# Kernel tuning notes

Hardware: AMD Instinct MI355X
Metric: run time of the kernel (lower is better)

Reference implementation:

```python
import jax, jax.numpy as jnp
import numpy as np

N_HEAD = 32
D_MODEL = 4096
N_KV_GROUPS = 8
D_HEAD = D_MODEL // N_HEAD            # 128
H_PER_G = N_HEAD // N_KV_GROUPS       # 4
KV_DIM = N_KV_GROUPS * D_HEAD         # 1024
B, S = 2, 2048


def setup_inputs() -> dict:
    key = jax.random.key(0)
    ks = jax.random.split(key, 8)
    q = jax.random.normal(ks[0], (B, S, D_MODEL), dtype=jnp.float32)
    k = jax.random.normal(ks[1], (B, S, D_MODEL), dtype=jnp.float32)
    v = jax.random.normal(ks[2], (B, S, D_MODEL), dtype=jnp.float32)
    # causal mask (True = keep), broadcast over b, g, h as in the torch module
    mask = jnp.tril(jnp.ones((S, S), dtype=bool))
    # params: torch init is torch.rand (uniform [0,1)); scale down for numerics
    w_q = jax.random.uniform(ks[3], (D_MODEL, D_MODEL), dtype=jnp.float32) * 0.02
    w_k = jax.random.uniform(ks[4], (KV_DIM, D_MODEL), dtype=jnp.float32) * 0.02
    w_v = jax.random.uniform(ks[5], (KV_DIM, D_MODEL), dtype=jnp.float32) * 0.02
    w_out = jax.random.uniform(ks[6], (D_MODEL, D_MODEL), dtype=jnp.float32) * 0.02
    return {"q": q, "k": k, "v": v, "w_q": w_q, "w_k": w_k, "w_v": w_v,
            "w_out": w_out, "mask": mask}


def reference(q, k, v, w_q, w_k, w_v, w_out, mask):
    b, n, _ = q.shape
    s = k.shape[1]
    # F.linear(x, W) == x @ W.T
    query = q @ w_q.T                                  # [b, n, d_model]
    key = k @ w_k.T                                    # [b, s, kv_dim]
    value = v @ w_v.T                                  # [b, s, kv_dim]
    # b n (h d) -> b h n d -> b g h n d
    query = query.reshape(b, n, N_HEAD, D_HEAD).transpose(0, 2, 1, 3)
    query = query.reshape(b, N_KV_GROUPS, H_PER_G, n, D_HEAD)
    # b s (g d) -> b g s d
    key = key.reshape(b, s, N_KV_GROUPS, D_HEAD).transpose(0, 2, 1, 3)
    value = value.reshape(b, s, N_KV_GROUPS, D_HEAD).transpose(0, 2, 1, 3)
    scores = jnp.einsum('bghnd,bgsd->bghns', query, key) / (D_HEAD ** 0.5)
    scores = jnp.where(mask, scores, jnp.finfo(scores.dtype).min)
    attention = jax.nn.softmax(scores, axis=-1)        # [b, g, h, n, s]
    out = jnp.einsum('bghns,bgsd->bghnd', attention, value)
    # b g h n d -> b n (g h d)
    out = out.transpose(0, 3, 1, 2, 4).reshape(b, n, D_MODEL)
    return out @ w_out.T
```

## Files before the change

### kernel.cpp

```cpp
#include <hip/hip_runtime.h>

typedef unsigned short u16;
typedef unsigned int u32;
typedef __bf16 bf16x8 __attribute__((ext_vector_type(8)));
typedef float f32x4 __attribute__((ext_vector_type(4)));
typedef u16 u16x8 __attribute__((ext_vector_type(8)));
typedef u32 u32x2 __attribute__((ext_vector_type(2)));

#define SCL2E 0.12751744898229718f

__device__ __forceinline__ u16 f2bf(float f) {
  union { float f; u32 u; } x; x.f = f;
  u32 r = x.u + 0x7fffu + ((x.u >> 16) & 1u);
  return (u16)(r >> 16);
}

__device__ __forceinline__ u32 cvt_pk_bf16(float lo, float hi) {
  u32 r;
  asm("v_cvt_pk_bf16_f32 %0, %1, %2" : "=v"(r) : "v"(lo), "v"(hi));
  return r;
}

__device__ __forceinline__ void gld16(const void* g, void* l) {
  __builtin_amdgcn_global_load_lds(
      (const __attribute__((address_space(1))) u32*)g,
      (__attribute__((address_space(3))) u32*)l, 16, 0, 0);
}

#define SBAR() __builtin_amdgcn_s_barrier()
#define WAITVM(N) do { asm volatile("s_waitcnt vmcnt(" #N ")" ::: "memory"); \
                       __builtin_amdgcn_sched_barrier(0); } while (0)

__device__ __forceinline__ void cvt_body(const float* __restrict__ in,
                                         u16* __restrict__ out, int n8) {
  int stride = gridDim.x * 256;
  for (int i = blockIdx.x * 256 + threadIdx.x; i < n8; i += stride) {
    float4 a = ((const float4*)in)[2*i];
    float4 b = ((const float4*)in)[2*i+1];
    u16x8 o;
    o[0]=f2bf(a.x); o[1]=f2bf(a.y); o[2]=f2bf(a.z); o[3]=f2bf(a.w);
    o[4]=f2bf(b.x); o[5]=f2bf(b.y); o[6]=f2bf(b.z); o[7]=f2bf(b.w);
    ((u16x8*)out)[i] = o;
  }
}

__global__ __launch_bounds__(256) void cvt3(
    const float* __restrict__ i0, const float* __restrict__ i1,
    const float* __restrict__ i2, u16* __restrict__ o0,
    u16* __restrict__ o1, u16* __restrict__ o2, int n8) {
  const float* in = blockIdx.y == 0 ? i0 : (blockIdx.y == 1 ? i1 : i2);
  u16* out = blockIdx.y == 0 ? o0 : (blockIdx.y == 1 ? o1 : o2);
  cvt_body(in, out, n8);
}

template<int OUTF32>
__device__ __forceinline__ void gemm256_body(
    const u16* __restrict__ Ag, const u16* __restrict__ Bg, void* __restrict__ Cp,
    const int K, const int ldc, const long m0, const long n0, const long cb,
    const float escale, u16* __restrict__ As, u16* __restrict__ Bs) {
  const int lane = threadIdx.x & 63, w = threadIdx.x >> 6;
  const int wm = w >> 2, wn = w & 3;
  const int c = lane & 15, grp = lane >> 4;
  const int lr = lane >> 3, lch = lane & 7;

  f32x4 acc[8][4] = {};
  const int NK = K >> 6;

#define STG(G, R0, DST, RIT, KT) do { \
    int rit_ = (RIT) + w*8 + lr; \
    int ch_ = lch ^ (rit_ & 7); \
    gld16((G) + ((R0) + rit_) * (long)K + (long)(KT)*64 + ch_*8, \
          (DST) + ((RIT) + w*8)*64); } while (0)

  STG(Bg, n0, Bs, 0, 0);   STG(Bg, n0, Bs, 64, 0);
  STG(Bg, n0, Bs, 128, 0); STG(Bg, n0, Bs, 192, 0);
  STG(Ag, m0, As, 0, 0);   STG(Ag, m0, As, 128, 0);
  STG(Ag, m0, As, 64, 0);  STG(Ag, m0, As, 192, 0);
  {
    u16* B1 = Bs + 16384;
    STG(Bg, n0, B1, 0, 1);   STG(Bg, n0, B1, 64, 1);
    STG(Bg, n0, B1, 128, 1); STG(Bg, n0, B1, 192, 1);
  }
  WAITVM(6);
  SBAR();

  for (int kt = 0; kt < NK; ++kt) {
    const u16* At = As + (kt & 1) * 16384;
    u16* An = As + ((kt & 1) ^ 1) * 16384;
    const u16* Bt = Bs + (kt % 3) * 16384;
    u16* Bn = Bs + ((kt + 2) % 3) * 16384;
    const bool am = (kt + 1 < NK), bm = (kt + 2 < NK);

    bf16x8 bfr[4][2];
#define LDAF(mi, ks) (*(const bf16x8*)(At + (wm*128 + (mi)*16 + c)*64 + ((((ks)*4 + grp)) ^ (c & 7))*8))
#define LDBF(ni, ks) (*(const bf16x8*)(Bt + (wn*64  + (ni)*16 + c)*64 + ((((ks)*4 + grp)) ^ (c & 7))*8))

#define PHASE(P, STAGES, WAITS) { \
    bf16x8 af0k0 = LDAF(2*(P),   0), af0k1 = LDAF(2*(P),   1); \
    bf16x8 af1k0 = LDAF(2*(P)+1, 0), af1k1 = LDAF(2*(P)+1, 1); \
    STAGES \
    WAITS \
    SBAR(); \
    __builtin_amdgcn_s_setprio(1); \
    _Pragma("unroll") \
    for (int ni = 0; ni < 4; ++ni) { \
      acc[2*(P)][ni]   = __builtin_amdgcn_mfma_f32_16x16x32_bf16(af0k0, bfr[ni][0], acc[2*(P)][ni],   0,0,0); \
      acc[2*(P)][ni]   = __builtin_amdgcn_mfma_f32_16x16x32_bf16(af0k1, bfr[ni][1], acc[2*(P)][ni],   0,0,0); \
      acc[2*(P)+1][ni] = __builtin_amdgcn_mfma_f32_16x16x32_bf16(af1k0, bfr[ni][0], acc[2*(P)+1][ni], 0,0,0); \
      acc[2*(P)+1][ni] = __builtin_amdgcn_mfma_f32_16x16x32_bf16(af1k1, bfr[ni][1], acc[2*(P)+1][ni], 0,0,0); \
    } \
    __builtin_amdgcn_s_setprio(0); \
    SBAR(); }

    #pragma unroll
    for (int ni = 0; ni < 4; ++ni) {
      bfr[ni][0] = LDBF(ni, 0);
      bfr[ni][1] = LDBF(ni, 1);
    }
    PHASE(0, if (am) { STG(Ag, m0, An, 0, kt+1); STG(Ag, m0, An, 128, kt+1); }, ;)
    PHASE(1, if (am) { STG(Ag, m0, An, 64, kt+1); STG(Ag, m0, An, 192, kt+1); },
             if (am) { WAITVM(4); } else { WAITVM(0); })
    PHASE(2, if (bm) { STG(Bg, n0, Bn, 0, kt+2); STG(Bg, n0, Bn, 64, kt+2); }, ;)
    PHASE(3, if (bm) { STG(Bg, n0, Bn, 128, kt+2); STG(Bg, n0, Bn, 192, kt+2); },
             if (bm) { WAITVM(6); } else if (am) { WAITVM(2); })
#undef PHASE
#undef LDAF
#undef LDBF
  }
#undef STG

  #pragma unroll
  for (int mi = 0; mi < 8; ++mi) {
    #pragma unroll
    for (int rr = 0; rr < 4; ++rr) {
      long row = m0 + wm*128 + mi*16 + grp*4 + rr;
      #pragma unroll
      for (int ni = 0; ni < 4; ++ni) {
        long col = cb + wn*64 + ni*16 + c;
        if (OUTF32) ((float*)Cp)[row*ldc + col] = acc[mi][ni][rr];
        else        ((u16*)Cp)[row*ldc + col]  = f2bf(acc[mi][ni][rr] * escale);
      }
    }
  }
}

__global__ __launch_bounds__(512, 2) void proj_gemm(
    const u16* __restrict__ qb, const u16* __restrict__ kb,
    const u16* __restrict__ vb, const u16* __restrict__ wqb,
    const u16* __restrict__ wkv, u16* __restrict__ Qp, u16* __restrict__ KVp) {
  __shared__ __attribute__((aligned(16))) u16 SMEM[5*16384];
  int wg = ((int)blockIdx.x & 7) * 48 + ((int)blockIdx.x >> 3);
  const u16 *A_, *B_; u16* C_; int ldc_; long m0, n0, cb; float esc;
  if (wg < 256)      { A_ = qb; B_ = wqb;           C_ = Qp;  ldc_ = 4096;
                       m0 = (long)(wg >> 4)*256; n0 = (long)(wg & 15)*256; cb = n0; esc = SCL2E; }
  else if (wg < 320) { int t = wg - 256; A_ = kb; B_ = wkv;   C_ = KVp; ldc_ = 2048;
                       m0 = (long)(t >> 2)*256; n0 = (long)(t & 3)*256; cb = n0; esc = 1.f; }
  else               { int t = wg - 320; A_ = vb; B_ = wkv + 4194304; C_ = KVp; ldc_ = 2048;
                       m0 = (long)(t >> 2)*256; n0 = (long)(t & 3)*256; cb = n0 + 1024; esc = 1.f; }
  gemm256_body<0>(A_, B_, C_, 4096, ldc_, m0, n0, cb, esc, SMEM, SMEM + 2*16384);
}

__global__ __launch_bounds__(512, 2) void gemm_out(
    const u16* __restrict__ A, const u16* __restrict__ Bw, float* __restrict__ C) {
  __shared__ __attribute__((aligned(16))) u16 SMEM[5*16384];
  int wg = ((int)blockIdx.x & 7) * 32 + ((int)blockIdx.x >> 3);
  long m0 = (long)(wg >> 4) * 256, n0 = (long)(wg & 15) * 256;
  gemm256_body<1>(A, Bw, C, 4096, 4096, m0, n0, n0, 1.f, SMEM, SMEM + 2*16384);
}

__global__ __launch_bounds__(256) void transpose_v(
    const u16* __restrict__ KVp, u16* __restrict__ Vt) {
  const int s0 = blockIdx.x * 64, n0 = blockIdx.y * 64, b = blockIdx.z;
  const int tid = threadIdx.x;
  __shared__ __attribute__((aligned(16))) u16 t[64*80];
  #pragma unroll
  for (int p = 0; p < 2; ++p) {
    int sl = p*32 + (tid >> 3), nl = (tid & 7) * 8;
    *(u16x8*)(t + sl*80 + nl) =
        *(const u16x8*)(KVp + (long)(b*2048 + s0 + sl)*2048 + 1024 + n0 + nl);
  }
  __syncthreads();
  #pragma unroll
  for (int p = 0; p < 2; ++p) {
    int nl = p*32 + (tid >> 3), sc = (tid & 7) * 8;
    u16x8 o;
    #pragma unroll
    for (int j = 0; j < 8; ++j) o[j] = t[(sc + j)*80 + nl];
    *(u16x8*)(Vt + (long)(b*1024 + n0 + nl)*2048 + s0 + sc) = o;
  }
}

__global__ __launch_bounds__(256, 2) void attn_fwd(
    const u16* __restrict__ Qp, const u16* __restrict__ KVp,
    const u16* __restrict__ Vt, u16* __restrict__ AO) {
  const int qt = gridDim.x - 1 - blockIdx.x;
  const int head = blockIdx.y, b = blockIdx.z;
  const int g = head >> 2;
  const int q0 = qt * 128;
  const int tid = threadIdx.x, lane = tid & 63, w = tid >> 6;
  const int c = lane & 15, grp = lane >> 4;
  const int qw = q0 + w * 32;

  __shared__ __attribute__((aligned(16))) u16 Ks[2][64*128];
  __shared__ __attribute__((aligned(16))) u16 Vts[2][128*64];
  __shared__ __attribute__((aligned(16))) u16 Ps[4][32*64];
  u16* __restrict__ pw = &Ps[w][0];

  bf16x8 qf[2][4];
  #pragma unroll
  for (int h = 0; h < 2; ++h) {
    const u16* qb = Qp + (long)(b*2048 + qw + h*16 + c)*4096 + head*128 + grp*8;
    #pragma unroll
    for (int t = 0; t < 4; ++t) qf[h][t] = *(const bf16x8*)(qb + t*32);
  }

  float m_run[2] = {-1e30f, -1e30f}, l_run[2] = {0.f, 0.f};
  f32x4 oacc[2][8] = {};

  const int ntiles = 2*qt + 2;

  auto STAGE = [&](int buf, int kt) {
    const int kv0 = kt * 64;
    #pragma unroll
    for (int p = 0; p < 4; ++p) {
      int idx = p*256 + w*64 + lane;
      int krow = idx >> 4, kc = idx & 15;
      int kcs = kc ^ (krow & 7);
      gld16(KVp + (long)(b*2048 + kv0 + krow)*2048 + g*128 + kcs*8,
            &Ks[buf][(p*256 + w*64)*8]);
      int d = idx >> 3, vc = idx & 7;
      int vcs = vc ^ (d & 7);
      gld16(Vt + (long)(b*1024 + g*128 + d)*2048 + kv0 + vcs*8,
            &Vts[buf][(p*256 + w*64)*8]);
    }
  };

  STAGE(0, 0);
  int cur = 0;
  for (int kt = 0; kt < ntiles; ++kt) {
    const int kv0 = kt * 64;
    __syncthreads();
    if (kt + 1 < ntiles) STAGE(cur ^ 1, kt + 1);

    const u16* __restrict__ Kc = &Ks[cur][0];
    const u16* __restrict__ Vc = &Vts[cur][0];

    f32x4 sacc[2][4] = {};
    #pragma unroll
    for (int f = 0; f < 4; ++f) {
      const int row = f*16 + c;
      #pragma unroll
      for (int t = 0; t < 4; ++t) {
        bf16x8 kf = *(const bf16x8*)(Kc + row*128 + (((t*4 + grp) ^ (c & 7)) * 8));
        sacc[0][f] = __builtin_amdgcn_mfma_f32_16x16x32_bf16(kf, qf[0][t], sacc[0][f], 0, 0, 0);
        sacc[1][f] = __builtin_amdgcn_mfma_f32_16x16x32_bf16(kf, qf[1][t], sacc[1][f], 0, 0, 0);
      }
    }

    #pragma unroll
    for (int h = 0; h < 2; ++h) {
      const int qg = qw + h*16 + c;
      float sv[16];
      if (kv0 + 63 > qw + h*16) {
        #pragma unroll
        for (int f = 0; f < 4; ++f)
          #pragma unroll
          for (int r = 0; r < 4; ++r) {
            float x = sacc[h][f][r];
            if (kv0 + f*16 + grp*4 + r > qg) x = -1e30f;
            sv[f*4 + r] = x;
          }
      } else {
        #pragma unroll
        for (int f = 0; f < 4; ++f)
          #pragma unroll
          for (int r = 0; r < 4; ++r) sv[f*4 + r] = sacc[h][f][r];
      }
      float tm[8];
      #pragma unroll
      for (int i = 0; i < 8; ++i) tm[i] = fmaxf(sv[i], sv[i+8]);
      #pragma unroll
      for (int i = 0; i < 4; ++i) tm[i] = fmaxf(tm[i], tm[i+4]);
      float tmax = fmaxf(fmaxf(tm[0], tm[2]), fmaxf(tm[1], tm[3]));
      tmax = fmaxf(tmax, __shfl_xor(tmax, 16));
      tmax = fmaxf(tmax, __shfl_xor(tmax, 32));

      float m_new = m_run[h];
      if (!__all(tmax <= m_run[h] + 8.f)) {
        m_new = fmaxf(m_run[h], tmax);
        float corr = exp2f(m_run[h] - m_new);
        l_run[h] *= corr;
        #pragma unroll
        for (int n = 0; n < 8; ++n) oacc[h][n] *= corr;
        m_run[h] = m_new;
      }

      float tsum = 0.f;
      u32 pk[8];
      #pragma unroll
      for (int i = 0; i < 8; ++i) {
        float p0 = exp2f(sv[2*i]   - m_new);
        float p1 = exp2f(sv[2*i+1] - m_new);
        tsum += p0 + p1;
        pk[i] = cvt_pk_bf16(p0, p1);
      }
      tsum += __shfl_xor(tsum, 16);
      tsum += __shfl_xor(tsum, 32);
      l_run[h] += tsum;

      #pragma unroll
      for (int f = 0; f < 4; ++f) {
        int col = (f*16 + grp*4) ^ ((c & 7) << 3);
        u32x2 pv; pv[0] = pk[2*f]; pv[1] = pk[2*f + 1];
        *(u32x2*)(pw + (h*16 + c)*64 + col) = pv;
      }
    }

    #pragma unroll
    for (int u = 0; u < 2; ++u) {
      const int pcol = (u*32 + grp*8) ^ ((c & 7) << 3);
      bf16x8 pf0 = *(const bf16x8*)(pw + c*64 + pcol);
      bf16x8 pf1 = *(const bf16x8*)(pw + (16 + c)*64 + pcol);
      #pragma unroll
      for (int n = 0; n < 8; ++n) {
        bf16x8 vf = *(const bf16x8*)(Vc + (n*16 + c)*64 + (((u*4 + grp) ^ (c & 7)) * 8));
        oacc[0][n] = __builtin_amdgcn_mfma_f32_16x16x32_bf16(vf, pf0, oacc[0][n], 0, 0, 0);
        oacc[1][n] = __builtin_amdgcn_mfma_f32_16x16x32_bf16(vf, pf1, oacc[1][n], 0, 0, 0);
      }
    }
    cur ^= 1;
  }

  #pragma unroll
  for (int h = 0; h < 2; ++h) {
    const float inv = 1.0f / l_run[h];
    u16* ob = AO + (long)(b*2048 + qw + h*16 + c)*4096 + head*128 + grp*4;
    #pragma unroll
    for (int n = 0; n < 8; ++n) {
      u32x2 o;
      o[0] = cvt_pk_bf16(oacc[h][n][0]*inv, oacc[h][n][1]*inv);
      o[1] = cvt_pk_bf16(oacc[h][n][2]*inv, oacc[h][n][3]*inv);
      *(u32x2*)(ob + n*16) = o;
    }
  }
}

extern "C" void kernel_launch(void* const* d_in, const int* in_sizes, int n_in,
                              void* d_out, int out_size, void* d_ws, size_t ws_size,
                              hipStream_t stream) {
  const float* q   = (const float*)d_in[0];
  const float* k   = (const float*)d_in[1];
  const float* v   = (const float*)d_in[2];
  const float* w_q = (const float*)d_in[3];
  const float* w_k = (const float*)d_in[4];
  const float* w_v = (const float*)d_in[5];
  const float* w_o = (const float*)d_in[6];

  u16* ws  = (u16*)d_ws;
  u16* qb  = ws;
  u16* kb  = qb  + 16777216;
  u16* vb  = kb  + 16777216;
  u16* wqb = vb  + 16777216;
  u16* wob = wqb + 16777216;
  u16* wkv = wob + 16777216;
  u16* Qp  = wkv + 8388608;
  u16* KVp = Qp  + 16777216;
  u16* Vtr = kb;
  u16* AO  = vb;
  (void)ws_size; (void)in_sizes; (void)n_in; (void)out_size;

  dim3 blk(256);
  cvt3<<<dim3(2048,3), blk, 0, stream>>>(q, k, v, qb, kb, vb, 2097152);
  cvt3<<<dim3(2048,2), blk, 0, stream>>>(w_q, w_o, w_o, wqb, wob, wob, 2097152);
  cvt3<<<dim3(512, 2), blk, 0, stream>>>(w_k, w_v, w_v, wkv, wkv + 4194304, wkv + 4194304, 524288);

  proj_gemm<<<384, dim3(512), 0, stream>>>(qb, kb, vb, wqb, wkv, Qp, KVp);
  transpose_v<<<dim3(32,16,2), blk, 0, stream>>>(KVp, Vtr);
  attn_fwd<<<dim3(16,32,2), blk, 0, stream>>>(Qp, KVp, Vtr, AO);
  gemm_out<<<256, dim3(512), 0, stream>>>(AO, wob, (float*)d_out);
}
```

Baseline: 629.7 us.

## Rebalance projection GEMM so each workgroup does one Q tile plus a K/V tile

The projection kernel used to launch 384 workgroups (256 Q tiles plus 128 K/V tiles of 256x256), which leaves a ragged second wave on 256 CUs. Now 256 workgroups each compute a 256x256 Q tile and then a 128x256 K or V tile through a new triple-buffered gemm128 body, so the per-workgroup work is even across a single wave. The attention kernel also raises wave priority around its MFMA blocks. The trade-offs are longer serial work per workgroup and LDS reuse between the two GEMMs in the same block. The final-phase wait logic in gemm256 is also slightly reshuffled.

```diff
diff --git a/kernel.cpp b/kernel.cpp
--- a/kernel.cpp
+++ b/kernel.cpp
@@ -30,6 +30,12 @@
 #define SBAR() __builtin_amdgcn_s_barrier()
 #define WAITVM(N) do { asm volatile("s_waitcnt vmcnt(" #N ")" ::: "memory"); \
                        __builtin_amdgcn_sched_barrier(0); } while (0)
+
+#define STG(G, R0, DST, RIT, KT, K) do { \
+    int rit_ = (RIT) + w*8 + lr; \
+    int ch_ = lch ^ (rit_ & 7); \
+    gld16((G) + ((R0) + rit_) * (long)(K) + (long)(KT)*64 + ch_*8, \
+          (DST) + ((RIT) + w*8)*64); } while (0)
 
 __device__ __forceinline__ void cvt_body(const float* __restrict__ in,
                                          u16* __restrict__ out, int n8) {
@@ -66,20 +72,14 @@
   f32x4 acc[8][4] = {};
   const int NK = K >> 6;
 
-#define STG(G, R0, DST, RIT, KT) do { \
-    int rit_ = (RIT) + w*8 + lr; \
-    int ch_ = lch ^ (rit_ & 7); \
-    gld16((G) + ((R0) + rit_) * (long)K + (long)(KT)*64 + ch_*8, \
-          (DST) + ((RIT) + w*8)*64); } while (0)
-
-  STG(Bg, n0, Bs, 0, 0);   STG(Bg, n0, Bs, 64, 0);
-  STG(Bg, n0, Bs, 128, 0); STG(Bg, n0, Bs, 192, 0);
-  STG(Ag, m0, As, 0, 0);   STG(Ag, m0, As, 128, 0);
-  STG(Ag, m0, As, 64, 0);  STG(Ag, m0, As, 192, 0);
+  STG(Bg, n0, Bs, 0, 0, K);   STG(Bg, n0, Bs, 64, 0, K);
+  STG(Bg, n0, Bs, 128, 0, K); STG(Bg, n0, Bs, 192, 0, K);
+  STG(Ag, m0, As, 0, 0, K);   STG(Ag, m0, As, 128, 0, K);
+  STG(Ag, m0, As, 64, 0, K);  STG(Ag, m0, As, 192, 0, K);
   {
     u16* B1 = Bs + 16384;
-    STG(Bg, n0, B1, 0, 1);   STG(Bg, n0, B1, 64, 1);
-    STG(Bg, n0, B1, 128, 1); STG(Bg, n0, B1, 192, 1);
+    STG(Bg, n0, B1, 0, 1, K);   STG(Bg, n0, B1, 64, 1, K);
+    STG(Bg, n0, B1, 128, 1, K); STG(Bg, n0, B1, 192, 1, K);
   }
   WAITVM(6);
   SBAR();
@@ -117,17 +117,16 @@
       bfr[ni][0] = LDBF(ni, 0);
       bfr[ni][1] = LDBF(ni, 1);
     }
-    PHASE(0, if (am) { STG(Ag, m0, An, 0, kt+1); STG(Ag, m0, An, 128, kt+1); }, ;)
-    PHASE(1, if (am) { STG(Ag, m0, An, 64, kt+1); STG(Ag, m0, An, 192, kt+1); },
+    PHASE(0, if (am) { STG(Ag, m0, An, 0, kt+1, K); STG(Ag, m0, An, 128, kt+1, K); }, ;)
+    PHASE(1, if (am) { STG(Ag, m0, An, 64, kt+1, K); STG(Ag, m0, An, 192, kt+1, K); },
              if (am) { WAITVM(4); } else { WAITVM(0); })
-    PHASE(2, if (bm) { STG(Bg, n0, Bn, 0, kt+2); STG(Bg, n0, Bn, 64, kt+2); }, ;)
-    PHASE(3, if (bm) { STG(Bg, n0, Bn, 128, kt+2); STG(Bg, n0, Bn, 192, kt+2); },
-             if (bm) { WAITVM(6); } else if (am) { WAITVM(2); })
+    PHASE(2, if (bm) { STG(Bg, n0, Bn, 0, kt+2, K); STG(Bg, n0, Bn, 64, kt+2, K); }, ;)
+    PHASE(3, if (bm) { STG(Bg, n0, Bn, 128, kt+2, K); STG(Bg, n0, Bn, 192, kt+2, K); WAITVM(6); }
+             else if (am) { WAITVM(2); }, ;)
 #undef PHASE
 #undef LDAF
 #undef LDBF
   }
-#undef STG
 
   #pragma unroll
   for (int mi = 0; mi < 8; ++mi) {
@@ -144,28 +143,112 @@
   }
 }
 
+__device__ __forceinline__ void gemm128_body(
+    const u16* __restrict__ Ag, const u16* __restrict__ Bg, u16* __restrict__ Cp,
+    const int K, const int ldc, const long m0, const long n0, const long cb,
+    u16* __restrict__ As, u16* __restrict__ Bs) {
+  const int lane = threadIdx.x & 63, w = threadIdx.x >> 6;
+  const int wm = w >> 2, wn = w & 3;
+  const int c = lane & 15, grp = lane >> 4;
+  const int lr = lane >> 3, lch = lane & 7;
+
+  f32x4 acc[4][4] = {};
+  const int NK = K >> 6;
+
+  STG(Bg, n0, Bs, 0, 0, K);   STG(Bg, n0, Bs, 64, 0, K);
+  STG(Bg, n0, Bs, 128, 0, K); STG(Bg, n0, Bs, 192, 0, K);
+  STG(Ag, m0, As, 0, 0, K);   STG(Ag, m0, As, 64, 0, K);
+  {
+    u16* B1 = Bs + 16384; u16* A1 = As + 8192;
+    STG(Bg, n0, B1, 0, 1, K);   STG(Bg, n0, B1, 64, 1, K);
+    STG(Bg, n0, B1, 128, 1, K); STG(Bg, n0, B1, 192, 1, K);
+    STG(Ag, m0, A1, 0, 1, K);   STG(Ag, m0, A1, 64, 1, K);
+  }
+  WAITVM(6);
+  SBAR();
+
+  for (int kt = 0; kt < NK; ++kt) {
+    const u16* At = As + (kt % 3) * 8192;
+    const u16* Bt = Bs + (kt % 3) * 16384;
+    u16* An = As + ((kt + 2) % 3) * 8192;
+    u16* Bn = Bs + ((kt + 2) % 3) * 16384;
+    const bool bm = (kt + 2 < NK);
+
+    bf16x8 bfr[4][2];
+#define LDAF(mi, ks) (*(const bf16x8*)(At + (wm*64 + (mi)*16 + c)*64 + ((((ks)*4 + grp)) ^ (c & 7))*8))
+#define LDBF(ni, ks) (*(const bf16x8*)(Bt + (wn*64 + (ni)*16 + c)*64 + ((((ks)*4 + grp)) ^ (c & 7))*8))
+
+#define PHASE2(P, STAGES, WAITS) { \
+    bf16x8 af0k0 = LDAF(2*(P),   0), af0k1 = LDAF(2*(P),   1); \
+    bf16x8 af1k0 = LDAF(2*(P)+1, 0), af1k1 = LDAF(2*(P)+1, 1); \
+    STAGES \
+    WAITS \
+    SBAR(); \
+    __builtin_amdgcn_s_setprio(1); \
+    _Pragma("unroll") \
+    for (int ni = 0; ni < 4; ++ni) { \
+      acc[2*(P)][ni]   = __builtin_amdgcn_mfma_f32_16x16x32_bf16(af0k0, bfr[ni][0], acc[2*(P)][ni],   0,0,0); \
+      acc[2*(P)][ni]   = __builtin_amdgcn_mfma_f32_16x16x32_bf16(af0k1, bfr[ni][1], acc[2*(P)][ni],   0,0,0); \
+      acc[2*(P)+1][ni] = __builtin_amdgcn_mfma_f32_16x16x32_bf16(af1k0, bfr[ni][0], acc[2*(P)+1][ni], 0,0,0); \
+      acc[2*(P)+1][ni] = __builtin_amdgcn_mfma_f32_16x16x32_bf16(af1k1, bfr[ni][1], acc[2*(P)+1][ni], 0,0,0); \
+    } \
+    __builtin_amdgcn_s_setprio(0); \
+    SBAR(); }
+
+    #pragma unroll
+    for (int ni = 0; ni < 4; ++ni) {
+      bfr[ni][0] = LDBF(ni, 0);
+      bfr[ni][1] = LDBF(ni, 1);
+    }
+    PHASE2(0, if (bm) { STG(Bg, n0, Bn, 0, kt+2, K); STG(Bg, n0, Bn, 64, kt+2, K); }, ;)
+    PHASE2(1, if (bm) { STG(Bg, n0, Bn, 128, kt+2, K); STG(Bg, n0, Bn, 192, kt+2, K);
+                        STG(Ag, m0, An, 0, kt+2, K); STG(Ag, m0, An, 64, kt+2, K); },
+              if (bm) { WAITVM(6); } else { WAITVM(0); })
+#undef PHASE2
+#undef LDAF
+#undef LDBF
+  }
+
+  #pragma unroll
+  for (int mi = 0; mi < 4; ++mi) {
+    #pragma unroll
+    for (int rr = 0; rr < 4; ++rr) {
+      long row = m0 + wm*64 + mi*16 + grp*4 + rr;
+      #pragma unroll
+      for (int ni = 0; ni < 4; ++ni) {
+        long col = cb + wn*64 + ni*16 + c;
+        Cp[row*ldc + col] = f2bf(acc[mi][ni][rr]);
+      }
+    }
+  }
+}
+
 __global__ __launch_bounds__(512, 2) void proj_gemm(
     const u16* __restrict__ qb, const u16* __restrict__ kb,
     const u16* __restrict__ vb, const u16* __restrict__ wqb,
     const u16* __restrict__ wkv, u16* __restrict__ Qp, u16* __restrict__ KVp) {
-  __shared__ __attribute__((aligned(16))) u16 SMEM[5*16384];
-  int wg = ((int)blockIdx.x & 7) * 48 + ((int)blockIdx.x >> 3);
-  const u16 *A_, *B_; u16* C_; int ldc_; long m0, n0, cb; float esc;
-  if (wg < 256)      { A_ = qb; B_ = wqb;           C_ = Qp;  ldc_ = 4096;
-                       m0 = (long)(wg >> 4)*256; n0 = (long)(wg & 15)*256; cb = n0; esc = SCL2E; }
-  else if (wg < 320) { int t = wg - 256; A_ = kb; B_ = wkv;   C_ = KVp; ldc_ = 2048;
-                       m0 = (long)(t >> 2)*256; n0 = (long)(t & 3)*256; cb = n0; esc = 1.f; }
-  else               { int t = wg - 320; A_ = vb; B_ = wkv + 4194304; C_ = KVp; ldc_ = 2048;
-                       m0 = (long)(t >> 2)*256; n0 = (long)(t & 3)*256; cb = n0 + 1024; esc = 1.f; }
-  gemm256_body<0>(A_, B_, C_, 4096, ldc_, m0, n0, cb, esc, SMEM, SMEM + 2*16384);
+  __shared__ __attribute__((aligned(16))) u16 SMEM[81920];
+  int wg = ((int)blockIdx.x & 7) * 32 + ((int)blockIdx.x >> 3);
+  gemm256_body<0>(qb, wqb, Qp, 4096, 4096,
+                  (long)(wg >> 4) * 256, (long)(wg & 15) * 256, (long)(wg & 15) * 256,
+                  SCL2E, SMEM, SMEM + 32768);
+  {
+    int mt = wg >> 3, nt = wg & 7;
+    const u16* A_ = (nt < 4) ? kb : vb;
+    const u16* B_ = wkv + ((nt < 4) ? 0 : 4194304);
+    long n0 = (long)(nt & 3) * 256;
+    long cb = (nt < 4) ? n0 : n0 + 1024;
+    gemm128_body(A_, B_, KVp, 4096, 2048, (long)mt * 128, n0, cb,
+                 SMEM, SMEM + 24576);
+  }
 }
 
 __global__ __launch_bounds__(512, 2) void gemm_out(
     const u16* __restrict__ A, const u16* __restrict__ Bw, float* __restrict__ C) {
-  __shared__ __attribute__((aligned(16))) u16 SMEM[5*16384];
+  __shared__ __attribute__((aligned(16))) u16 SMEM[81920];
   int wg = ((int)blockIdx.x & 7) * 32 + ((int)blockIdx.x >> 3);
   long m0 = (long)(wg >> 4) * 256, n0 = (long)(wg & 15) * 256;
-  gemm256_body<1>(A, Bw, C, 4096, 4096, m0, n0, n0, 1.f, SMEM, SMEM + 2*16384);
+  gemm256_body<1>(A, Bw, C, 4096, 4096, m0, n0, n0, 1.f, SMEM, SMEM + 32768);
 }
 
 __global__ __launch_bounds__(256) void transpose_v(
@@ -246,6 +329,7 @@
     const u16* __restrict__ Vc = &Vts[cur][0];
 
     f32x4 sacc[2][4] = {};
+    __builtin_amdgcn_s_setprio(1);
     #pragma unroll
     for (int f = 0; f < 4; ++f) {
       const int row = f*16 + c;
@@ -256,6 +340,7 @@
         sacc[1][f] = __builtin_amdgcn_mfma_f32_16x16x32_bf16(kf, qf[1][t], sacc[1][f], 0, 0, 0);
       }
     }
+    __builtin_amdgcn_s_setprio(0);
 
     #pragma unroll
     for (int h = 0; h < 2; ++h) {
@@ -316,6 +401,7 @@
       }
     }
 
+    __builtin_amdgcn_s_setprio(1);
     #pragma unroll
     for (int u = 0; u < 2; ++u) {
       const int pcol = (u*32 + grp*8) ^ ((c & 7) << 3);
@@ -328,6 +414,7 @@
         oacc[1][n] = __builtin_amdgcn_mfma_f32_16x16x32_bf16(vf, pf1, oacc[1][n], 0, 0, 0);
       }
     }
+    __builtin_amdgcn_s_setprio(0);
     cur ^= 1;
   }
 
@@ -374,7 +461,7 @@
   cvt3<<<dim3(2048,2), blk, 0, stream>>>(w_q, w_o, w_o, wqb, wob, wob, 2097152);
   cvt3<<<dim3(512, 2), blk, 0, stream>>>(w_k, w_v, w_v, wkv, wkv + 4194304, wkv + 4194304, 524288);
 
-  proj_gemm<<<384, dim3(512), 0, stream>>>(qb, kb, vb, wqb, wkv, Qp, KVp);
+  proj_gemm<<<256, dim3(512), 0, stream>>>(qb, kb, vb, wqb, wkv, Qp, KVp);
   transpose_v<<<dim3(32,16,2), blk, 0, stream>>>(KVp, Vtr);
   attn_fwd<<<dim3(16,32,2), blk, 0, stream>>>(Qp, KVp, Vtr, AO);
   gemm_out<<<256, dim3(512), 0, stream>>>(AO, wob, (float*)d_out);
```

After: 612.6 us. 2.7% less time.
